# Kernel tuning notes

Hardware: AMD Instinct MI355X
Metric: run time of the kernel (lower is better)

## Reference

```python
import jax, jax.numpy as jnp
import numpy as np
from jax import lax

STRIDE = 2
PAD = 1
EPS = 1e-6
K = 2  # top-k experts
E = 4  # num_experts
B, C1, H, W = 32, 64, 64, 64
C2 = 128
PATCH = 3


def conv_ln(x, w, b, gamma, beta):
    # Conv2d(c1->c2, patch, stride, pad) followed by channel-first LayerNorm
    y = lax.conv_general_dilated(x, w, (STRIDE, STRIDE), ((PAD, PAD), (PAD, PAD)),
                                 dimension_numbers=('NCHW', 'OIHW', 'NCHW'))
    y = y + b[None, :, None, None]
    u = y.mean(1, keepdims=True)
    s = ((y - u) ** 2).mean(1, keepdims=True)
    y = (y - u) / jnp.sqrt(s + EPS)
    return gamma[None, :, None, None] * y + beta[None, :, None, None]


def setup_inputs() -> dict:
    key = jax.random.key(0)
    ks = jax.random.split(key, 10)
    x = jax.random.normal(ks[0], (B, C1, H, W), dtype=jnp.float32)
    w_gate = jax.random.normal(ks[1], (C1, E), dtype=jnp.float32) * 0.02
    expert_w = jax.random.normal(ks[2], (E, C2, C1, PATCH, PATCH), dtype=jnp.float32) * 0.05
    expert_b = jax.random.normal(ks[3], (E, C2), dtype=jnp.float32) * 0.01
    expert_ln_w = jnp.ones((E, C2), dtype=jnp.float32)
    expert_ln_b = jnp.zeros((E, C2), dtype=jnp.float32)
    shared_w = jax.random.normal(ks[4], (C2, C1, PATCH, PATCH), dtype=jnp.float32) * 0.05
    shared_b = jax.random.normal(ks[5], (C2,), dtype=jnp.float32) * 0.01
    shared_ln_w = jnp.ones((C2,), dtype=jnp.float32)
    shared_ln_b = jnp.zeros((C2,), dtype=jnp.float32)
    return {"x": x, "w_gate": w_gate,
            "expert_w": expert_w, "expert_b": expert_b,
            "expert_ln_w": expert_ln_w, "expert_ln_b": expert_ln_b,
            "shared_w": shared_w, "shared_b": shared_b,
            "shared_ln_w": shared_ln_w, "shared_ln_b": shared_ln_b}


def reference(x, w_gate, expert_w, expert_b, expert_ln_w, expert_ln_b,
              shared_w, shared_b, shared_ln_w, shared_ln_b):
    # --- noisy top-k gating (eval mode: no noise) ---
    gate_in = x.mean(axis=(2, 3))            # [B, width]
    logits = gate_in @ w_gate                # [B, E]
    top_vals, top_idx = lax.top_k(logits, K) # [B, K]
    top_gates = jax.nn.softmax(top_vals, axis=-1)
    # scatter top-k gate values back to dense [B, E] gate matrix
    gates = jnp.sum(jax.nn.one_hot(top_idx, E, dtype=x.dtype) * top_gates[..., None], axis=1)
    # --- per-expert conv+LN; dense-weighted combine is math-equivalent to
    #     SparseDispatcher dispatch -> expert -> weighted index_add combine ---
    expert_out = jax.vmap(lambda w, b, g, bt: conv_ln(x, w, b, g, bt))(
        expert_w, expert_b, expert_ln_w, expert_ln_b)   # [E, B, C2, H', W']
    combined = jnp.einsum('be,ebchw->bchw', gates, expert_out)
    # --- shared expert added to routed output ---
    shared = conv_ln(x, shared_w, shared_b, shared_ln_w, shared_ln_b)
    return combined + shared
```

## Files before the change

### kernel.cpp

```cpp
#include <hip/hip_runtime.h>
#include <cstdint>
#include <cstddef>

#define NB    32
#define NC1   64
#define NC2   128
#define NE    4
#define NSLOT 5
#define HIN   64
#define WIN   64
#define HOUT  32
#define WOUT  32

#define GATEIN_OFF 0
#define BIAS_OFF   2176
#define GAMMA_OFF  2816
#define BETA_OFF   3456
#define WBF_OFF    4096

typedef __bf16 bf16x8 __attribute__((ext_vector_type(8)));
typedef float  f32x16 __attribute__((ext_vector_type(16)));

__global__ void prep2_kernel(const float* __restrict__ x,
                             const float* __restrict__ expert_w,
                             const float* __restrict__ shared_w,
                             const float* __restrict__ expert_b,
                             const float* __restrict__ shared_b,
                             const float* __restrict__ eln_w,
                             const float* __restrict__ sln_w,
                             const float* __restrict__ eln_b,
                             const float* __restrict__ sln_b,
                             float* __restrict__ ws) {
    int bid = blockIdx.x;
    if (bid < 1440) {
        int i = bid * 256 + threadIdx.x;
        {
            int j    = i & 7;
            int l    = (i >> 3) & 63;
            int kk   = (i >> 9) & 3;
            int wv   = (i >> 11) & 3;
            int rest = i >> 13;
            int tap  = rest % 9;
            int e    = rest / 9;
            int c2 = wv * 32 + (l & 31);
            int c  = kk * 16 + (l >> 5) * 8 + j;
            float v;
            if (e < NE) v = expert_w[(((size_t)(e * NC2 + c2) * NC1 + c) * 9) + tap];
            else        v = shared_w[(((size_t)c2 * NC1 + c) * 9) + tap];
            ((__bf16*)(ws + WBF_OFF))[i] = (__bf16)v;
        }
        if (i < NSLOT * NC2) {
            int e = i >> 7, c2 = i & 127;
            ws[BIAS_OFF  + i] = (e < NE) ? expert_b[i] : shared_b[c2];
            ws[GAMMA_OFF + i] = (e < NE) ? eln_w[i]    : sln_w[c2];
            ws[BETA_OFF  + i] = (e < NE) ? eln_b[i]    : sln_b[c2];
        }
    } else {
        int row  = (bid - 1440) * 4 + (threadIdx.x >> 6);
        int lane = threadIdx.x & 63;
        const float* src = x + (size_t)row * (HIN * WIN);
        float s = 0.f;
        for (int i = lane * 4; i < HIN * WIN; i += 64 * 4) {
            float4 v = *(const float4*)(src + i);
            s += v.x + v.y + v.z + v.w;
        }
        #pragma unroll
        for (int off = 32; off >= 1; off >>= 1) s += __shfl_xor(s, off);
        if (lane == 0) ws[GATEIN_OFF + row] = s * (1.f / (HIN * WIN));
    }
}

#define XS_IDX(r, p, ps, c7) ((((r) * 65 + (p)) << 6) + ((ps) << 3) + (c7))

__global__ __launch_bounds__(512, 2) void fused_kernel(
        const float* __restrict__ x,
        const float* __restrict__ w_gate,
        const float* __restrict__ ws,
        float* __restrict__ out) {
    __shared__ __bf16 xs[9 * 65 * 64];
    __shared__ float  red[3 * 2 * 2 * 2 * 128];

    const int bid = blockIdx.x;
    const int b   = bid >> 3;
    const int q   = bid & 7;
    const int tid = threadIdx.x;
    const int ln  = tid & 63;
    const int wv8 = tid >> 6;
    const int tg  = wv8 >> 2;
    const int wv  = wv8 & 3;
    const int cl  = ln & 31;
    const int hl  = ln >> 5;
    const int wbase = wv * 32;

    int s0, s1; float ga, gb;
    {
        float gi = ws[GATEIN_OFF + b * NC1 + ln];
        float l[NE];
        #pragma unroll
        for (int e = 0; e < NE; ++e) {
            float p = gi * w_gate[ln * NE + e];
            #pragma unroll
            for (int off = 32; off >= 1; off >>= 1) p += __shfl_xor(p, off);
            l[e] = p;
        }
        int i0 = 0; float v0 = l[0];
        #pragma unroll
        for (int e = 1; e < NE; ++e) if (l[e] > v0) { v0 = l[e]; i0 = e; }
        int i1 = -1; float v1 = -3.4e38f;
        #pragma unroll
        for (int e = 0; e < NE; ++e) if (e != i0 && l[e] > v1) { v1 = l[e]; i1 = e; }
        float e1 = expf(v1 - v0);
        float denom = 1.f + e1;
        s0 = i0; ga = 1.f / denom;
        s1 = i1; gb = e1 / denom;
    }

    const __bf16* wtab = (const __bf16*)(ws + WBF_OFF);
    const __bf16* ap0 = wtab + (size_t)s0 * 73728 + wv * 2048 + ln * 8;
    const __bf16* ap1 = wtab + (size_t)s1 * 73728 + wv * 2048 + ln * 8;
    const __bf16* ap2 = wtab + (size_t)4  * 73728 + wv * 2048 + ln * 8;

    bf16x8 A0[12], A1[12];
    #define LOAD_A(DST, TAP)                                                      \
    {                                                                             \
        _Pragma("unroll")                                                         \
        for (int kk = 0; kk < 4; ++kk) {                                          \
            DST[kk]     = *(const bf16x8*)(ap0 + (TAP) * 8192 + kk * 512);        \
            DST[4 + kk] = *(const bf16x8*)(ap1 + (TAP) * 8192 + kk * 512);        \
            DST[8 + kk] = *(const bf16x8*)(ap2 + (TAP) * 8192 + kk * 512);        \
        }                                                                         \
    }
    LOAD_A(A0, 0)

    #pragma unroll
    for (int pass = 0; pass < 18; ++pass) {
        int idx = pass * 512 + tid;
        int r   = idx >> 10;
        int rem = idx & 1023;
        int c   = rem >> 4;
        int i4  = rem & 15;
        int hin = 8 * q - 1 + r;
        float4 v = make_float4(0.f, 0.f, 0.f, 0.f);
        if (hin >= 0)
            v = *(const float4*)(x + (((size_t)b * NC1 + c) * HIN + hin) * WIN + i4 * 4);
        #pragma unroll
        for (int k = 0; k < 4; ++k) {
            int p  = i4 * 4 + k + 1;
            int ps = (c >> 3) ^ ((p >> 1) & 7);
            float f = (k == 0) ? v.x : (k == 1) ? v.y : (k == 2) ? v.z : v.w;
            xs[XS_IDX(r, p, ps, c & 7)] = (__bf16)f;
        }
    }
    if (tid < 64) {
        #pragma unroll
        for (int r = 0; r < 9; ++r) xs[XS_IDX(r, 0, (tid >> 3), tid & 7)] = (__bf16)0.f;
    }

    const int rowbase = wbase + 4 * hl;
    f32x16 c00, c01, c10, c11, c20, c21;
    #define INIT_ACC(ACC, SID)                                                  \
    {                                                                           \
        const float4* bp = (const float4*)(ws + BIAS_OFF + (SID) * NC2 + rowbase); \
        float4 b0 = bp[0], b1 = bp[2], b2 = bp[4], b3 = bp[6];                  \
        ACC[0]=b0.x; ACC[1]=b0.y; ACC[2]=b0.z; ACC[3]=b0.w;                     \
        ACC[4]=b1.x; ACC[5]=b1.y; ACC[6]=b1.z; ACC[7]=b1.w;                     \
        ACC[8]=b2.x; ACC[9]=b2.y; ACC[10]=b2.z; ACC[11]=b2.w;                   \
        ACC[12]=b3.x; ACC[13]=b3.y; ACC[14]=b3.z; ACC[15]=b3.w;                 \
    }
    INIT_ACC(c00, s0) c01 = c00;
    INIT_ACC(c10, s1) c11 = c10;
    INIT_ACC(c20, 4)  c21 = c20;

    __syncthreads();

    #define MFMA(A, B, C) C = __builtin_amdgcn_mfma_f32_32x32x16_bf16(A, B, C, 0, 0, 0)
    const int p_l = 2 * cl;
    #define COMPUTE(A, TAP)                                                       \
    {                                                                             \
        const int r3  = (TAP) / 3;                                                \
        const int kw  = (TAP) % 3;                                                \
        const int p   = p_l + kw;                                                 \
        const int swb = (p >> 1) & 7;                                             \
        const int rA  = 4 * tg + r3;                                              \
        const int rB  = rA + 2;                                                   \
        bf16x8 bA0 = *(const bf16x8*)&xs[XS_IDX(rA, p, (0 + hl) ^ swb, 0)];       \
        bf16x8 bA1 = *(const bf16x8*)&xs[XS_IDX(rA, p, (2 + hl) ^ swb, 0)];       \
        bf16x8 bA2 = *(const bf16x8*)&xs[XS_IDX(rA, p, (4 + hl) ^ swb, 0)];       \
        bf16x8 bA3 = *(const bf16x8*)&xs[XS_IDX(rA, p, (6 + hl) ^ swb, 0)];       \
        bf16x8 bB0 = *(const bf16x8*)&xs[XS_IDX(rB, p, (0 + hl) ^ swb, 0)];       \
        bf16x8 bB1 = *(const bf16x8*)&xs[XS_IDX(rB, p, (2 + hl) ^ swb, 0)];       \
        bf16x8 bB2 = *(const bf16x8*)&xs[XS_IDX(rB, p, (4 + hl) ^ swb, 0)];       \
        bf16x8 bB3 = *(const bf16x8*)&xs[XS_IDX(rB, p, (6 + hl) ^ swb, 0)];       \
        MFMA(A[0], bA0, c00); MFMA(A[0], bB0, c01);                               \
        MFMA(A[1], bA1, c00); MFMA(A[1], bB1, c01);                               \
        MFMA(A[2], bA2, c00); MFMA(A[2], bB2, c01);                               \
        MFMA(A[3], bA3, c00); MFMA(A[3], bB3, c01);                               \
        MFMA(A[4], bA0, c10); MFMA(A[4], bB0, c11);                               \
        MFMA(A[5], bA1, c10); MFMA(A[5], bB1, c11);                               \
        MFMA(A[6], bA2, c10); MFMA(A[6], bB2, c11);                               \
        MFMA(A[7], bA3, c10); MFMA(A[7], bB3, c11);                               \
        MFMA(A[8], bA0, c20); MFMA(A[8], bB0, c21);                               \
        MFMA(A[9], bA1, c20); MFMA(A[9], bB1, c21);                               \
        MFMA(A[10], bA2, c20); MFMA(A[10], bB2, c21);                             \
        MFMA(A[11], bA3, c20); MFMA(A[11], bB3, c21);                             \
    }
    LOAD_A(A1, 1)  COMPUTE(A0, 0)  LOAD_A(A0, 2)  COMPUTE(A1, 1)
    LOAD_A(A1, 3)  COMPUTE(A0, 2)  LOAD_A(A0, 4)  COMPUTE(A1, 3)
    LOAD_A(A1, 5)  COMPUTE(A0, 4)  LOAD_A(A0, 6)  COMPUTE(A1, 5)
    LOAD_A(A1, 7)  COMPUTE(A0, 6)  LOAD_A(A0, 8)  COMPUTE(A1, 7)
    COMPUTE(A0, 8)

    #define PUT_RED(ACC, SI, U)                                                   \
    {                                                                             \
        float sum = 0.f, sq = 0.f;                                                \
        _Pragma("unroll")                                                         \
        for (int i = 0; i < 16; ++i) { float a = ACC[i]; sum += a; sq += a * a; } \
        sum += __shfl_xor(sum, 32); sq += __shfl_xor(sq, 32);                     \
        if (ln < 32) {                                                            \
            red[((((SI) * 2 + tg) * 2 + (U)) * 2 + 0) * 128 + wbase + cl] = sum;  \
            red[((((SI) * 2 + tg) * 2 + (U)) * 2 + 1) * 128 + wbase + cl] = sq;   \
        }                                                                         \
    }
    PUT_RED(c00, 0, 0) PUT_RED(c01, 0, 1)
    PUT_RED(c10, 1, 0) PUT_RED(c11, 1, 1)
    PUT_RED(c20, 2, 0) PUT_RED(c21, 2, 1)
    __syncthreads();

    float fin0[16], fin1[16];
    #pragma unroll
    for (int i = 0; i < 16; ++i) { fin0[i] = 0.f; fin1[i] = 0.f; }

    #define APPLY(ACC, FIN, SI, U, GM, BT, G)                                     \
    {                                                                             \
        float tot = 0.f, totq = 0.f;                                              \
        _Pragma("unroll")                                                         \
        for (int w = 0; w < 4; ++w) {                                             \
            tot  += red[((((SI) * 2 + tg) * 2 + (U)) * 2 + 0) * 128 + w * 32 + cl]; \
            totq += red[((((SI) * 2 + tg) * 2 + (U)) * 2 + 1) * 128 + w * 32 + cl]; \
        }                                                                         \
        float mean = tot * (1.f / NC2);                                           \
        float var  = totq * (1.f / NC2) - mean * mean;                            \
        float rstd = rsqrtf(var + 1e-6f);                                         \
        _Pragma("unroll")                                                         \
        for (int i = 0; i < 16; ++i) {                                            \
            float nrm = (ACC[i] - mean) * rstd;                                   \
            FIN[i] = fmaf((G), fmaf(GM[i], nrm, BT[i]), FIN[i]);                  \
        }                                                                         \
    }
    #define LOAD_GB(SID, GM, BT)                                                  \
        float GM[16], BT[16];                                                     \
        {                                                                         \
            const float4* gmp = (const float4*)(ws + GAMMA_OFF + (SID) * NC2 + rowbase); \
            const float4* btp = (const float4*)(ws + BETA_OFF  + (SID) * NC2 + rowbase); \
            float4 g0 = gmp[0], g1 = gmp[2], g2 = gmp[4], g3 = gmp[6];            \
            float4 t0 = btp[0], t1 = btp[2], t2 = btp[4], t3 = btp[6];            \
            GM[0]=g0.x;GM[1]=g0.y;GM[2]=g0.z;GM[3]=g0.w;GM[4]=g1.x;GM[5]=g1.y;GM[6]=g1.z;GM[7]=g1.w; \
            GM[8]=g2.x;GM[9]=g2.y;GM[10]=g2.z;GM[11]=g2.w;GM[12]=g3.x;GM[13]=g3.y;GM[14]=g3.z;GM[15]=g3.w; \
            BT[0]=t0.x;BT[1]=t0.y;BT[2]=t0.z;BT[3]=t0.w;BT[4]=t1.x;BT[5]=t1.y;BT[6]=t1.z;BT[7]=t1.w; \
            BT[8]=t2.x;BT[9]=t2.y;BT[10]=t2.z;BT[11]=t2.w;BT[12]=t3.x;BT[13]=t3.y;BT[14]=t3.z;BT[15]=t3.w; \
        }
    {
        LOAD_GB(s0, gm0, bt0)
        APPLY(c00, fin0, 0, 0, gm0, bt0, ga)
        APPLY(c01, fin1, 0, 1, gm0, bt0, ga)
    }
    {
        LOAD_GB(s1, gm1, bt1)
        APPLY(c10, fin0, 1, 0, gm1, bt1, gb)
        APPLY(c11, fin1, 1, 1, gm1, bt1, gb)
    }
    {
        LOAD_GB(4, gm2, bt2)
        APPLY(c20, fin0, 2, 0, gm2, bt2, 1.0f)
        APPLY(c21, fin1, 2, 1, gm2, bt2, 1.0f)
    }

    {
        const int hp0 = 4 * q + 2 * tg;
        float* ob = out + (size_t)b * (NC2 * HOUT * WOUT) + hp0 * WOUT + cl;
        #pragma unroll
        for (int i = 0; i < 16; ++i) {
            int c2 = rowbase + (i & 3) + 8 * (i >> 2);
            ob[(size_t)c2 * (HOUT * WOUT)] = fin0[i];
            ob[(size_t)c2 * (HOUT * WOUT) + WOUT] = fin1[i];
        }
    }
}

extern "C" void kernel_launch(void* const* d_in, const int* in_sizes, int n_in,
                              void* d_out, int out_size, void* d_ws, size_t ws_size,
                              hipStream_t stream) {
    const float* x        = (const float*)d_in[0];
    const float* w_gate   = (const float*)d_in[1];
    const float* expert_w = (const float*)d_in[2];
    const float* expert_b = (const float*)d_in[3];
    const float* eln_w    = (const float*)d_in[4];
    const float* eln_b    = (const float*)d_in[5];
    const float* shared_w = (const float*)d_in[6];
    const float* shared_b = (const float*)d_in[7];
    const float* sln_w    = (const float*)d_in[8];
    const float* sln_b    = (const float*)d_in[9];
    float* ws  = (float*)d_ws;
    float* out = (float*)d_out;

    prep2_kernel<<<1952, 256, 0, stream>>>(x, expert_w, shared_w, expert_b, shared_b,
                                           eln_w, sln_w, eln_b, sln_b, ws);
    fused_kernel<<<NB * 8, 512, 0, stream>>>(x, w_gate, ws, out);
}
```

Baseline: 39.22 us.

## Pre-transpose x to channel-last bf16 and stage via global_load_lds

The prep kernel now transposes x into an NHWC bf16 table in workspace and computes gate means with atomics. The fused kernel then fills its LDS input tile with direct global-to-LDS DMA loads in place of per-thread float4 loads, conversion and scattered bf16 stores. Zero padding comes from a small zeroed workspace buffer. This adds an extra full pass writing x in bf16, two memsets and atomics, in exchange for cheaper staging in the main kernel.

```diff
diff --git a/kernel.cpp b/kernel.cpp
--- a/kernel.cpp
+++ b/kernel.cpp
@@ -16,10 +16,21 @@
 #define BIAS_OFF   2176
 #define GAMMA_OFF  2816
 #define BETA_OFF   3456
-#define WBF_OFF    4096
+#define ZPAD_OFF   4096
+#define WBF_OFF    4128
+#define XT_OFF     188448
 
 typedef __bf16 bf16x8 __attribute__((ext_vector_type(8)));
 typedef float  f32x16 __attribute__((ext_vector_type(16)));
+
+#define GLOAD_LDS16(G, L)                                                        \
+    __builtin_amdgcn_global_load_lds(                                            \
+        (const __attribute__((address_space(1))) void*)(G),                      \
+        (__attribute__((address_space(3))) void*)(L), 16, 0, 0)
+#define GLOAD_LDS4(G, L)                                                         \
+    __builtin_amdgcn_global_load_lds(                                            \
+        (const __attribute__((address_space(1))) void*)(G),                      \
+        (__attribute__((address_space(3))) void*)(L), 4, 0, 0)
 
 __global__ void prep2_kernel(const float* __restrict__ x,
                              const float* __restrict__ expert_w,
@@ -31,6 +42,7 @@
                              const float* __restrict__ eln_b,
                              const float* __restrict__ sln_b,
                              float* __restrict__ ws) {
+    __shared__ float tile[64 * 65];
     int bid = blockIdx.x;
     if (bid < 1440) {
         int i = bid * 256 + threadIdx.x;
@@ -56,28 +68,47 @@
             ws[BETA_OFF  + i] = (e < NE) ? eln_b[i]    : sln_b[c2];
         }
     } else {
-        int row  = (bid - 1440) * 4 + (threadIdx.x >> 6);
-        int lane = threadIdx.x & 63;
-        const float* src = x + (size_t)row * (HIN * WIN);
-        float s = 0.f;
-        for (int i = lane * 4; i < HIN * WIN; i += 64 * 4) {
-            float4 v = *(const float4*)(src + i);
-            s += v.x + v.y + v.z + v.w;
-        }
-        #pragma unroll
-        for (int off = 32; off >= 1; off >>= 1) s += __shfl_xor(s, off);
-        if (lane == 0) ws[GATEIN_OFF + row] = s * (1.f / (HIN * WIN));
+        int tb = bid - 1440;
+        int b  = tb >> 6, h = tb & 63;
+        int t  = threadIdx.x;
+        int c  = t >> 2, wq = t & 3;
+        const float* src = x + (((size_t)b * NC1 + c) * HIN + h) * WIN + wq * 16;
+        float4 v0 = ((const float4*)src)[0];
+        float4 v1 = ((const float4*)src)[1];
+        float4 v2 = ((const float4*)src)[2];
+        float4 v3 = ((const float4*)src)[3];
+        float* tr = &tile[c * 65 + wq * 16];
+        tr[0]=v0.x; tr[1]=v0.y; tr[2]=v0.z; tr[3]=v0.w;
+        tr[4]=v1.x; tr[5]=v1.y; tr[6]=v1.z; tr[7]=v1.w;
+        tr[8]=v2.x; tr[9]=v2.y; tr[10]=v2.z; tr[11]=v2.w;
+        tr[12]=v3.x; tr[13]=v3.y; tr[14]=v3.z; tr[15]=v3.w;
+        float s = v0.x+v0.y+v0.z+v0.w + v1.x+v1.y+v1.z+v1.w
+                + v2.x+v2.y+v2.z+v2.w + v3.x+v3.y+v3.z+v3.w;
+        s += __shfl_xor(s, 1);
+        s += __shfl_xor(s, 2);
+        if (wq == 0) atomicAdd(&ws[GATEIN_OFF + b * NC1 + c], s * (1.f / 4096.f));
+        __syncthreads();
+        int w = t >> 2, cq = t & 3;
+        bf16x8 o0, o1;
+        #pragma unroll
+        for (int j = 0; j < 8; ++j) o0[j] = (__bf16)tile[(cq * 16 + j) * 65 + w];
+        #pragma unroll
+        for (int j = 0; j < 8; ++j) o1[j] = (__bf16)tile[(cq * 16 + 8 + j) * 65 + w];
+        __bf16* dst = (__bf16*)(ws + XT_OFF)
+                      + ((((size_t)b * 64 + h) * 64 + w) * 64 + cq * 16);
+        *(bf16x8*)dst = o0;
+        *((bf16x8*)dst + 1) = o1;
     }
 }
 
-#define XS_IDX(r, p, ps, c7) ((((r) * 65 + (p)) << 6) + ((ps) << 3) + (c7))
+#define XS_IDX(r, p, ps, c7) ((((r) * 66 + (p)) << 6) + ((ps) << 3) + (c7))
 
 __global__ __launch_bounds__(512, 2) void fused_kernel(
         const float* __restrict__ x,
         const float* __restrict__ w_gate,
         const float* __restrict__ ws,
         float* __restrict__ out) {
-    __shared__ __bf16 xs[9 * 65 * 64];
+    __shared__ __bf16 xs[9 * 66 * 64];
     __shared__ float  red[3 * 2 * 2 * 2 * 128];
 
     const int bid = blockIdx.x;
@@ -132,28 +163,30 @@
     }
     LOAD_A(A0, 0)
 
-    #pragma unroll
-    for (int pass = 0; pass < 18; ++pass) {
-        int idx = pass * 512 + tid;
-        int r   = idx >> 10;
-        int rem = idx & 1023;
-        int c   = rem >> 4;
-        int i4  = rem & 15;
-        int hin = 8 * q - 1 + r;
-        float4 v = make_float4(0.f, 0.f, 0.f, 0.f);
-        if (hin >= 0)
-            v = *(const float4*)(x + (((size_t)b * NC1 + c) * HIN + hin) * WIN + i4 * 4);
-        #pragma unroll
-        for (int k = 0; k < 4; ++k) {
-            int p  = i4 * 4 + k + 1;
-            int ps = (c >> 3) ^ ((p >> 1) & 7);
-            float f = (k == 0) ? v.x : (k == 1) ? v.y : (k == 2) ? v.z : v.w;
-            xs[XS_IDX(r, p, ps, c & 7)] = (__bf16)f;
-        }
-    }
-    if (tid < 64) {
-        #pragma unroll
-        for (int r = 0; r < 9; ++r) xs[XS_IDX(r, 0, (tid >> 3), tid & 7)] = (__bf16)0.f;
+    {
+        const __bf16* xtab = (const __bf16*)(ws + XT_OFF);
+        const __bf16* zp   = (const __bf16*)(ws + ZPAD_OFF);
+        for (int ii = wv8; ii < 81; ii += 8) {
+            int r   = ii / 9;
+            int u   = ii - r * 9;
+            int hin = 8 * q - 1 + r;
+            const __bf16* xrow = xtab + (((size_t)b * 64 + hin) * 64) * 64;
+            if (u < 8) {
+                int pbase = u << 3;
+                int p   = pbase + (ln >> 3);
+                int swb = (p >> 1) & 7;
+                int cblk = ((ln & 7) ^ swb) << 3;
+                const __bf16* src = (hin >= 0 && p >= 1)
+                                    ? (xrow + (size_t)(p - 1) * 64 + cblk) : zp;
+                GLOAD_LDS16(src, &xs[(r * 66 + pbase) << 6]);
+            } else {
+                int p = 64 + (ln >> 5);
+                int c = (((ln >> 2) & 7) << 3) + 2 * (ln & 3);
+                const __bf16* src = (hin >= 0 && p == 64)
+                                    ? (xrow + (size_t)63 * 64 + c) : zp;
+                GLOAD_LDS4(src, &xs[(r * 66 + 64) << 6]);
+            }
+        }
     }
 
     const int rowbase = wbase + 4 * hl;
@@ -303,7 +336,10 @@
     float* ws  = (float*)d_ws;
     float* out = (float*)d_out;
 
-    prep2_kernel<<<1952, 256, 0, stream>>>(x, expert_w, shared_w, expert_b, shared_b,
+    hipMemsetAsync(ws + GATEIN_OFF, 0, NB * NC1 * sizeof(float), stream);
+    hipMemsetAsync(ws + ZPAD_OFF, 0, 32 * sizeof(float), stream);
+
+    prep2_kernel<<<3488, 256, 0, stream>>>(x, expert_w, shared_w, expert_b, shared_b,
                                            eln_w, sln_w, eln_b, sln_b, ws);
     fused_kernel<<<NB * 8, 512, 0, stream>>>(x, w_gate, ws, out);
 }
```

Result: slower. 44.69 us (+14.0%).
